# Kernel tuning notes

Measured on AMD Instinct MI355X. Metric: run time of the kernel, lower is better.

## Reference

```python
import jax, jax.numpy as jnp
import numpy as np

B, T = 16, 2048
NEG = -1e9  # finite large-negative for masked softmax (avoids NaN on empty rows)


def setup_inputs() -> dict:
    key = jax.random.key(0)
    k1, k2 = jax.random.split(key)
    logits = jax.random.normal(k1, (B, T, 1), dtype=jnp.float32)
    seq_len = jax.random.randint(k2, (B,), 1, T + 1, dtype=jnp.int32)
    return {"logits": logits, "seq_len": seq_len}


def reference(logits, seq_len):
    scores = jax.nn.sigmoid(logits.squeeze(-1))  # [B, T]
    # pairwise relevance: sigmoid((1 - |s_i - s_j| - 0.5) / 0.1)
    pairwise_diff = scores[:, :, None] - scores[:, None, :]  # [B, T, T]
    rel_mat = jax.nn.sigmoid((1.0 - jnp.abs(pairwise_diff) - 0.5) / 0.1)
    # ragged mask: valid positions are < seq_len[b]
    valid = jnp.arange(T)[None, :] < seq_len[:, None]            # [B, T]
    mask2d = valid[:, :, None] & valid[:, None, :]               # [B, T, T]
    masked = jnp.where(mask2d, rel_mat, NEG)
    sm = jax.nn.softmax(masked, axis=-1)                          # masked cols -> ~0
    # zero out invalid rows (original leaves them as zeros)
    out_mat = jnp.where(valid[:, :, None], sm, 0.0)
    return out_mat
```

## Files before the change

### kernel.cpp

```cpp
#include <hip/hip_runtime.h>

#define TT 2048
#define BLOCK 256
#define ROWS 8

__device__ __forceinline__ float fast_sigmoid(float x) {
    return __builtin_amdgcn_rcpf(1.0f + __expf(-x));
}

__global__ __launch_bounds__(BLOCK) void score_branch_kernel(
    const float* __restrict__ logits, const int* __restrict__ seq_len,
    float* __restrict__ out)
{
    __shared__ float s_scores[TT];
    __shared__ float s_red[BLOCK / 64];

    const int b    = blockIdx.y;
    const int row0 = blockIdx.x * ROWS;
    const int tid  = threadIdx.x;
    const int L    = seq_len[b];

    const float4* lg4 = (const float4*)(logits + (size_t)b * TT);
    float4* s4 = (float4*)s_scores;
    #pragma unroll
    for (int k = 0; k < TT / (BLOCK * 4); ++k) {
        int idx4 = tid + k * BLOCK;
        float4 v = lg4[idx4];
        float4 s;
        s.x = fast_sigmoid(v.x);
        s.y = fast_sigmoid(v.y);
        s.z = fast_sigmoid(v.z);
        s.w = fast_sigmoid(v.w);
        s4[idx4] = s;
    }
    __syncthreads();

    const int lane = tid & 63;
    const int wv   = tid >> 6;

    for (int r = 0; r < ROWS; ++r) {
        const int i = row0 + r;
        float4* orow4 = (float4*)(out + ((size_t)b * TT + (size_t)i) * TT);

        if (i >= L) {
            float4 z = make_float4(0.f, 0.f, 0.f, 0.f);
            #pragma unroll
            for (int k = 0; k < TT / (BLOCK * 4); ++k)
                orow4[tid + k * BLOCK] = z;
            continue;
        }

        const float si = s_scores[i];
        float e[2][4];
        float partial = 0.f;
        #pragma unroll
        for (int k = 0; k < 2; ++k) {
            int idx4 = tid + k * BLOCK;
            float4 sj = s4[idx4];
            float vals[4] = {sj.x, sj.y, sj.z, sj.w};
            int j0 = idx4 * 4;
            #pragma unroll
            for (int q = 0; q < 4; ++q) {
                float d  = si - vals[q];
                float t  = fmaf(fabsf(d), -10.0f, 5.0f);
                float p  = fast_sigmoid(t);
                float ee = __expf(p);
                ee = (j0 + q < L) ? ee : 0.0f;
                e[k][q] = ee;
                partial += ee;
            }
        }

        #pragma unroll
        for (int off = 32; off > 0; off >>= 1)
            partial += __shfl_xor(partial, off, 64);
        if (lane == 0) s_red[wv] = partial;
        __syncthreads();
        float total = s_red[0] + s_red[1] + s_red[2] + s_red[3];
        float inv = __builtin_amdgcn_rcpf(total);

        #pragma unroll
        for (int k = 0; k < 2; ++k) {
            int idx4 = tid + k * BLOCK;
            float4 o;
            o.x = e[k][0] * inv;
            o.y = e[k][1] * inv;
            o.z = e[k][2] * inv;
            o.w = e[k][3] * inv;
            orow4[idx4] = o;
        }
        __syncthreads();
    }
}

extern "C" void kernel_launch(void* const* d_in, const int* in_sizes, int n_in,
                              void* d_out, int out_size, void* d_ws, size_t ws_size,
                              hipStream_t stream) {
    const float* logits  = (const float*)d_in[0];
    const int*   seq_len = (const int*)d_in[1];
    float*       out     = (float*)d_out;

    const int B = in_sizes[1];
    dim3 grid(TT / ROWS, B);
    score_branch_kernel<<<grid, dim3(BLOCK), 0, stream>>>(logits, seq_len, out);
}
```

Baseline: 258.7 us.

## Assign one row per wavefront and drop block-level reduction barriers

Each wavefront now owns a whole output row, so the softmax sum is reduced with wave shuffles alone and the shared-memory reduction and per-row __syncthreads are removed. Blocks handle 4 rows instead of 8, so the grid is twice as large and the score table is loaded and run through sigmoid more times per row. Each lane keeps 32 exp values in registers, which raises register pressure.

```diff
diff --git a/kernel.cpp b/kernel.cpp
--- a/kernel.cpp
+++ b/kernel.cpp
@@ -2,7 +2,7 @@
 
 #define TT 2048
 #define BLOCK 256
-#define ROWS 8
+#define WAVES (BLOCK / 64)
 
 __device__ __forceinline__ float fast_sigmoid(float x) {
     return __builtin_amdgcn_rcpf(1.0f + __expf(-x));
@@ -13,11 +13,12 @@
     float* __restrict__ out)
 {
     __shared__ float s_scores[TT];
-    __shared__ float s_red[BLOCK / 64];
 
     const int b    = blockIdx.y;
-    const int row0 = blockIdx.x * ROWS;
+    const int row0 = blockIdx.x * WAVES;
     const int tid  = threadIdx.x;
+    const int lane = tid & 63;
+    const int wv   = tid >> 6;
     const int L    = seq_len[b];
 
     const float4* lg4 = (const float4*)(logits + (size_t)b * TT);
@@ -35,61 +36,53 @@
     }
     __syncthreads();
 
-    const int lane = tid & 63;
-    const int wv   = tid >> 6;
+    const int i = row0 + wv;
+    float4* orow4 = (float4*)(out + ((size_t)b * TT + (size_t)i) * TT);
 
-    for (int r = 0; r < ROWS; ++r) {
-        const int i = row0 + r;
-        float4* orow4 = (float4*)(out + ((size_t)b * TT + (size_t)i) * TT);
+    if (i >= L) {
+        float4 z = make_float4(0.f, 0.f, 0.f, 0.f);
+        #pragma unroll
+        for (int q = 0; q < 8; ++q)
+            orow4[q * 64 + lane] = z;
+        return;
+    }
 
-        if (i >= L) {
-            float4 z = make_float4(0.f, 0.f, 0.f, 0.f);
-            #pragma unroll
-            for (int k = 0; k < TT / (BLOCK * 4); ++k)
-                orow4[tid + k * BLOCK] = z;
-            continue;
+    const float si = s_scores[i];
+
+    float4 e4[8];
+    float partial = 0.f;
+    #pragma unroll
+    for (int q = 0; q < 8; ++q) {
+        const int idx4 = q * 64 + lane;
+        float4 sj = s4[idx4];
+        const int j0 = idx4 * 4;
+        float vals[4] = {sj.x, sj.y, sj.z, sj.w};
+        float* ev = (float*)&e4[q];
+        #pragma unroll
+        for (int qq = 0; qq < 4; ++qq) {
+            float d  = si - vals[qq];
+            float t  = fmaf(fabsf(d), -10.0f, 5.0f);
+            float p  = fast_sigmoid(t);
+            float ee = __expf(p);
+            ee = (j0 + qq < L) ? ee : 0.0f;
+            ev[qq] = ee;
+            partial += ee;
         }
+    }
 
-        const float si = s_scores[i];
-        float e[2][4];
-        float partial = 0.f;
-        #pragma unroll
-        for (int k = 0; k < 2; ++k) {
-            int idx4 = tid + k * BLOCK;
-            float4 sj = s4[idx4];
-            float vals[4] = {sj.x, sj.y, sj.z, sj.w};
-            int j0 = idx4 * 4;
-            #pragma unroll
-            for (int q = 0; q < 4; ++q) {
-                float d  = si - vals[q];
-                float t  = fmaf(fabsf(d), -10.0f, 5.0f);
-                float p  = fast_sigmoid(t);
-                float ee = __expf(p);
-                ee = (j0 + q < L) ? ee : 0.0f;
-                e[k][q] = ee;
-                partial += ee;
-            }
-        }
+    #pragma unroll
+    for (int off = 32; off > 0; off >>= 1)
+        partial += __shfl_xor(partial, off, 64);
+    const float inv = __builtin_amdgcn_rcpf(partial);
 
-        #pragma unroll
-        for (int off = 32; off > 0; off >>= 1)
-            partial += __shfl_xor(partial, off, 64);
-        if (lane == 0) s_red[wv] = partial;
-        __syncthreads();
-        float total = s_red[0] + s_red[1] + s_red[2] + s_red[3];
-        float inv = __builtin_amdgcn_rcpf(total);
-
-        #pragma unroll
-        for (int k = 0; k < 2; ++k) {
-            int idx4 = tid + k * BLOCK;
-            float4 o;
-            o.x = e[k][0] * inv;
-            o.y = e[k][1] * inv;
-            o.z = e[k][2] * inv;
-            o.w = e[k][3] * inv;
-            orow4[idx4] = o;
-        }
-        __syncthreads();
+    #pragma unroll
+    for (int q = 0; q < 8; ++q) {
+        float4 o;
+        o.x = e4[q].x * inv;
+        o.y = e4[q].y * inv;
+        o.z = e4[q].z * inv;
+        o.w = e4[q].w * inv;
+        orow4[q * 64 + lane] = o;
     }
 }
 
@@ -101,6 +94,6 @@
     float*       out     = (float*)d_out;
 
     const int B = in_sizes[1];
-    dim3 grid(TT / ROWS, B);
+    dim3 grid(TT / WAVES, B);
     score_branch_kernel<<<grid, dim3(BLOCK), 0, stream>>>(logits, seq_len, out);
 }
```

After: 257.7 us (median of 2 runs). Within noise of the previous version (-0.4%).
